# Kernel tuning notes

Hardware: AMD Instinct MI355X
Metric: run time of the kernel (lower is better)

The kernel has to match this reference:

```python
import jax, jax.numpy as jnp
import numpy as np
from jax import lax

DN = ('NHWC', 'HWIO', 'NHWC')

def conv2d_same(x, W, b):
    y = lax.conv_general_dilated(x, W, window_strides=(1, 1), padding='SAME', dimension_numbers=DN)
    return y + b

def maxpool2(x):
    # 2x2 max pool, stride 2, SAME padding (NHWC)
    return lax.reduce_window(x, -jnp.inf, lax.max, (1, 2, 2, 1), (1, 2, 2, 1), 'SAME')

def setup_inputs() -> dict:
    key = jax.random.key(0)
    ks = jax.random.split(key, 6)
    B, H, W, C = 8, 64, 64, 256
    s = 0.05
    return {
        'x': jax.random.normal(ks[0], (B, H, W, C), jnp.float32),
        'Wf': jax.random.normal(ks[1], (3, 3, C, C // 8), jnp.float32) * s,
        'bf': jnp.zeros((C // 8,), jnp.float32),
        'Wg': jax.random.normal(ks[2], (3, 3, C, C // 8), jnp.float32) * s,
        'bg': jnp.zeros((C // 8,), jnp.float32),
        'Wh': jax.random.normal(ks[3], (3, 3, C, C // 2), jnp.float32) * s,
        'bh': jnp.zeros((C // 2,), jnp.float32),
        'Wo': jax.random.normal(ks[4], (1, 1, C // 2, C), jnp.float32) * s,
        'bo': jnp.zeros((C,), jnp.float32),
        'gate': jnp.ones((1,), jnp.float32),
    }

def reference(x, Wf, bf, Wg, bg, Wh, bh, Wo, bo, gate):
    B, H, W, C = x.shape
    f = maxpool2(conv2d_same(x, Wf, bf))            # [B, H/2, W/2, C//8] keys
    g = conv2d_same(x, Wg, bg)                       # [B, H, W, C//8]     queries
    h = maxpool2(conv2d_same(x, Wh, bh))            # [B, H/2, W/2, C//2] values
    N, M = H * W, (H // 2) * (W // 2)
    gq = g.reshape(B, N, C // 8)
    fk = f.reshape(B, M, C // 8)
    hv = h.reshape(B, M, C // 2)
    attn = jax.nn.softmax(jnp.einsum('bnd,bmd->bnm', gq, fk), axis=-1)  # [B, N, M]
    wo = jnp.einsum('bnm,bmv->bnv', attn, hv).reshape(B, H, W, C // 2)
    out = conv2d_same(wo, Wo, bo)                    # [B, H, W, C]
    return x + gate[0] * out
```

## Files before the change

kernel.cpp:

```cpp
#include <hip/hip_runtime.h>
#include <hip/hip_fp16.h>

constexpr int B_  = 8;
constexpr int H_  = 64;
constexpr int W_  = 64;
constexpr int C_  = 256;
constexpr int CG_ = 32;
constexpr int CH_ = 128;
constexpr int NQ_ = 4096;
constexpr int NM_ = 1024;
constexpr int XP_ = 66;

constexpr int GP_ = 1048576;
constexpr int HP_ = 4194304;

typedef __attribute__((ext_vector_type(8))) _Float16 half8;
typedef __attribute__((ext_vector_type(4))) _Float16 half4;
typedef __attribute__((ext_vector_type(4))) float    f32x4;

__global__ void prep_w_k(const float* __restrict__ Wg, const float* __restrict__ Wf,
                         const float* __restrict__ Wh, const float* __restrict__ Wo,
                         const float* __restrict__ bg, const float* __restrict__ bf,
                         const float* __restrict__ bh,
                         _Float16* __restrict__ Wpk, _Float16* __restrict__ Wok,
                         float* __restrict__ bc) {
    int i = blockIdx.x * 256 + threadIdx.x;
    if (i < 12 * 9 * 8 * 64 * 8) {
        int j    = i & 7;
        int lane = (i >> 3) & 63;
        int ks   = (i >> 9) & 7;
        int tap  = (i >> 12) % 9;
        int co16 = i / 36864;
        int co = co16 * 16 + (lane & 15);
        int kk = tap * 256 + ks * 32 + (lane >> 4) * 8 + j;
        float v;
        if (co < 32)      v = Wg[(size_t)kk * 32  + co];
        else if (co < 64) v = Wf[(size_t)kk * 32  + (co - 32)];
        else              v = Wh[(size_t)kk * 128 + (co - 64)];
        Wpk[i] = (_Float16)v;
        return;
    }
    int i2 = i - 12 * 9 * 8 * 64 * 8;
    if (i2 < 16 * 4 * 64 * 8) {
        int j    = i2 & 7;
        int lane = (i2 >> 3) & 63;
        int ks   = (i2 >> 9) & 3;
        int co16 = i2 >> 11;
        int co = co16 * 16 + (lane & 15);
        int k  = ks * 32 + (lane >> 4) * 8 + j;
        Wok[i2] = (_Float16)Wo[(size_t)k * 256 + co];
        return;
    }
    int co = i2 - 16 * 4 * 64 * 8;
    if (co < 192)
        bc[co] = (co < 32) ? bg[co] : (co < 64) ? bf[co - 32] : bh[co - 64];
}

__global__ __launch_bounds__(256, 4) void conv_mfma_k(
        const float* __restrict__ X, const _Float16* __restrict__ Wpk,
        const float* __restrict__ bc,
        _Float16* __restrict__ gpart, _Float16* __restrict__ fpart,
        _Float16* __restrict__ hpart) {
    __shared__ char lds[XP_ * 256 * 2];
    int bid = blockIdx.x;
    int lg  = (bid & 7) * 192 + (bid >> 3);
    int ky  = lg % 3;
    int iy  = lg / 3;
    int b   = iy >> 6;
    int y   = iy & 63;
    int yy  = y + ky - 1;
    int tid = threadIdx.x;
    int wid = tid >> 6;
    int l   = tid & 63;
    int lr  = l & 15;
    int lk  = l >> 4;

    {
        bool rowok = (yy >= 0 && yy < 64);
        const float* xrow = X + ((size_t)(b * 64 + yy) * 64) * 256;
        half8 vst[9];
#pragma unroll
        for (int j = 0; j < 9; ++j) {
            int c = tid + j * 256;
            half8 v = (half8)(_Float16)0.f;
            if (j < 8 || tid < 64) {
                int px = c >> 5;
                int ch = (c & 31) * 8;
                if (rowok && px >= 1 && px <= 64) {
                    const float* s = xrow + (size_t)(px - 1) * 256 + ch;
                    float4 a  = *reinterpret_cast<const float4*>(s);
                    float4 b2 = *reinterpret_cast<const float4*>(s + 4);
                    v[0] = (_Float16)a.x;  v[1] = (_Float16)a.y;
                    v[2] = (_Float16)a.z;  v[3] = (_Float16)a.w;
                    v[4] = (_Float16)b2.x; v[5] = (_Float16)b2.y;
                    v[6] = (_Float16)b2.z; v[7] = (_Float16)b2.w;
                }
            }
            vst[j] = v;
        }
#pragma unroll
        for (int j = 0; j < 9; ++j) {
            int c = tid + j * 256;
            if (j < 8 || tid < 64) {
                int px = c >> 5;
                *reinterpret_cast<half8*>(lds + ((c * 16) ^ ((px & 7) << 4))) = vst[j];
            }
        }
    }
    __syncthreads();

    f32x4 acc[4][3];
#pragma unroll
    for (int mi = 0; mi < 4; ++mi)
#pragma unroll
        for (int nj = 0; nj < 3; ++nj) acc[mi][nj] = (f32x4)0.f;

    int tap0 = ky * 3;
    auto ldw = [&](int s, half8* d) {
        const _Float16* p = Wpk +
            ((((size_t)(wid * 3) * 9 + tap0 + (s >> 3)) * 8 + (s & 7)) * 64 + l) * 8;
        d[0] = *reinterpret_cast<const half8*>(p);
        d[1] = *reinterpret_cast<const half8*>(p + 36864);
        d[2] = *reinterpret_cast<const half8*>(p + 73728);
    };

    half8 wb[3][3];
    ldw(0, wb[0]);
    ldw(1, wb[1]);
#pragma unroll
    for (int st = 0; st < 24; ++st) {
        if (st < 22) ldw(st + 2, wb[(st + 2) % 3]);
        int kx = st >> 3, ks = st & 7;
        half8 af[4];
#pragma unroll
        for (int mi = 0; mi < 4; ++mi) {
            int px = mi * 16 + lr + kx;
            int ad = (px * 512 + ks * 64 + lk * 16) ^ ((px & 7) << 4);
            af[mi] = *reinterpret_cast<const half8*>(lds + ad);
        }
        const half8* w = wb[st % 3];
#pragma unroll
        for (int mi = 0; mi < 4; ++mi)
            acc[mi][0] = __builtin_amdgcn_mfma_f32_16x16x32_f16(af[mi], w[0], acc[mi][0], 0, 0, 0);
#pragma unroll
        for (int mi = 0; mi < 4; ++mi)
            acc[mi][1] = __builtin_amdgcn_mfma_f32_16x16x32_f16(af[mi], w[1], acc[mi][1], 0, 0, 0);
#pragma unroll
        for (int mi = 0; mi < 4; ++mi)
            acc[mi][2] = __builtin_amdgcn_mfma_f32_16x16x32_f16(af[mi], w[2], acc[mi][2], 0, 0, 0);
    }

    int pixbase = (b * 64 + y) * 64;
    bool addb = (ky == 1);
#pragma unroll
    for (int nj = 0; nj < 3; ++nj) {
        int co = wid * 48 + nj * 16 + lr;
        float bias = addb ? bc[co] : 0.f;
#pragma unroll
        for (int mi = 0; mi < 4; ++mi) {
#pragma unroll
            for (int r = 0; r < 4; ++r) {
                int x = mi * 16 + lk * 4 + r;
                float v = acc[mi][nj][r] + bias;
                size_t pix = pixbase + x;
                if (co < 32)
                    gpart[(size_t)ky * GP_ + pix * 32 + co] = (_Float16)(v * 1.44269504f);
                else if (co < 64)
                    fpart[(size_t)ky * GP_ + pix * 32 + (co - 32)] = (_Float16)v;
                else
                    hpart[(size_t)ky * HP_ + pix * 128 + (co - 64)] = (_Float16)v;
            }
        }
    }
}

__global__ void maxpool_f16_k(const _Float16* __restrict__ fp, _Float16* __restrict__ dst) {
    int i = blockIdx.x * 256 + threadIdx.x;
    if (i >= B_ * NM_ * CG_) return;
    int c = i & 31;
    int t = i >> 5;
    int px = t & 31;
    int py = (t >> 5) & 31;
    int b  = t >> 10;
    size_t base = (((size_t)(b * 64 + py * 2)) * 64 + px * 2) * 32 + c;
    const _Float16* p1 = fp + GP_;
    const _Float16* p2 = fp + 2 * GP_;
    auto val = [&](size_t o) { return (float)fp[o] + (float)p1[o] + (float)p2[o]; };
    float v = fmaxf(fmaxf(val(base), val(base + 32)),
                    fmaxf(val(base + 64 * 32), val(base + 64 * 32 + 32)));
    dst[i] = (_Float16)v;
}

__global__ __launch_bounds__(256) void vtpool_k(const _Float16* __restrict__ hp,
                                                _Float16* __restrict__ Vt) {
    __shared__ float t[32][33];
    int b  = blockIdx.x >> 7;
    int kt = (blockIdx.x >> 2) & 31;
    int ct = blockIdx.x & 3;
    int tid = threadIdx.x;
    const _Float16* p1 = hp + HP_;
    const _Float16* p2 = hp + 2 * (size_t)HP_;
#pragma unroll
    for (int i = 0; i < 4; ++i) {
        int e = tid + i * 256;
        int px = e >> 5, c = e & 31;
        size_t base = (((size_t)(b * 64 + kt * 2) * 64) + px * 2) * 128 + ct * 32 + c;
        auto val = [&](size_t o) { return (float)hp[o] + (float)p1[o] + (float)p2[o]; };
        float v = fmaxf(fmaxf(val(base), val(base + 128)),
                        fmaxf(val(base + 64 * 128), val(base + 64 * 128 + 128)));
        t[px][c] = v;
    }
    __syncthreads();
#pragma unroll
    for (int i = 0; i < 4; ++i) {
        int e = tid + i * 256;
        int c = e >> 5, px = e & 31;
        Vt[((size_t)b * 128 + ct * 32 + c) * 1024 + kt * 32 + px] = (_Float16)t[px][c];
    }
}

constexpr int PP_ = 72;

__global__ __launch_bounds__(256, 2) void attn_flash_k(
        const _Float16* __restrict__ Qp,
        const _Float16* __restrict__ Kf,
        const _Float16* __restrict__ Vt,
        _Float16* __restrict__ wo) {
    __shared__ _Float16 plds[4][16][PP_];
    __shared__ _Float16 vlds[2][8192];
    int bb  = blockIdx.x >> 6;
    int qt  = blockIdx.x & 63;
    int wid = threadIdx.x >> 6;
    int l   = threadIdx.x & 63;
    int lr  = l & 15;
    int lg  = l >> 4;
    int qbase = qt * 64 + wid * 16;

    const _Float16* gp = Qp + ((size_t)bb * NQ_ + qbase + lr) * 32 + lg * 8;
    half8 bq = *reinterpret_cast<const half8*>(gp);
    bq = bq + *reinterpret_cast<const half8*>(gp + GP_);
    bq = bq + *reinterpret_cast<const half8*>(gp + 2 * GP_);

    const _Float16* Kb = Kf + (size_t)bb * NM_ * 32;
    const _Float16* Vb = Vt + (size_t)bb * 128 * NM_;

    int o0  = wid * 4096 + l * 16;
    int vr0 = o0 >> 7;
    int vc  = (o0 >> 4) & 7;
    int vsw = (vr0 & 7) << 4;
    int lsw = (lr & 7) << 4;

    f32x4 acc[8];
#pragma unroll
    for (int vt = 0; vt < 8; ++vt) acc[vt] = (f32x4)0.f;
    float m_run = -1.0e30f;
    float l_lane = 0.f;

    half8 ak0, ak1, ak2, ak3;
    f32x4 s0, s1, s2, s3;
    half4 ph0, ph1, ph2, ph3;
    float4 vst[4];

#define STAGE_LOAD(T)                                                              \
    {   const _Float16* vp = Vb + (size_t)(T) * 64 + (size_t)vr0 * NM_ + vc * 8;   \
        vst[0] = *reinterpret_cast<const float4*>(vp);                             \
        vst[1] = *reinterpret_cast<const float4*>(vp + 8 * NM_);                   \
        vst[2] = *reinterpret_cast<const float4*>(vp + 16 * NM_);                  \
        vst[3] = *reinterpret_cast<const float4*>(vp + 24 * NM_);                  \
    }

#define STAGE_WRITE(BUF)                                                           \
    {   char* vbp = (char*)vlds[BUF] + (o0 ^ vsw);                                 \
        *reinterpret_cast<float4*>(vbp)        = vst[0];                           \
        *reinterpret_cast<float4*>(vbp + 1024) = vst[1];                           \
        *reinterpret_cast<float4*>(vbp + 2048) = vst[2];                           \
        *reinterpret_cast<float4*>(vbp + 3072) = vst[3];                           \
    }

#define LOADK(T)                                                                   \
    {   const _Float16* kp = Kb + (size_t)(T) * 64 * 32;                           \
        ak0 = *reinterpret_cast<const half8*>(kp + (size_t)(lr)      * 32 + lg*8); \
        ak1 = *reinterpret_cast<const half8*>(kp + (size_t)(16 + lr) * 32 + lg*8); \
        ak2 = *reinterpret_cast<const half8*>(kp + (size_t)(32 + lr) * 32 + lg*8); \
        ak3 = *reinterpret_cast<const half8*>(kp + (size_t)(48 + lr) * 32 + lg*8); \
    }

#define QK()                                                                \
    {   s0 = __builtin_amdgcn_mfma_f32_16x16x32_f16(ak0, bq, (f32x4)0.f, 0, 0, 0); \
        s1 = __builtin_amdgcn_mfma_f32_16x16x32_f16(ak1, bq, (f32x4)0.f, 0, 0, 0); \
        s2 = __builtin_amdgcn_mfma_f32_16x16x32_f16(ak2, bq, (f32x4)0.f, 0, 0, 0); \
        s3 = __builtin_amdgcn_mfma_f32_16x16x32_f16(ak3, bq, (f32x4)0.f, 0, 0, 0); \
    }

#define SOFTMAX()                                                           \
    {   float lm = fmaxf(fmaxf(fmaxf(s0[0], s0[1]), fmaxf(s0[2], s0[3])),   \
                         fmaxf(fmaxf(s1[0], s1[1]), fmaxf(s1[2], s1[3])));  \
        lm = fmaxf(lm, fmaxf(fmaxf(fmaxf(s2[0], s2[1]), fmaxf(s2[2], s2[3])), \
                             fmaxf(fmaxf(s3[0], s3[1]), fmaxf(s3[2], s3[3])))); \
        if (__any(lm > m_run + 11.0f)) {                                    \
            float mx = lm;                                                  \
            mx = fmaxf(mx, __shfl_xor(mx, 16, 64));                         \
            mx = fmaxf(mx, __shfl_xor(mx, 32, 64));                         \
            float mnew  = fmaxf(m_run, mx);                                 \
            float alpha = exp2f(m_run - mnew);                              \
            l_lane *= alpha;                                                \
            _Pragma("unroll")                                               \
            for (int r = 0; r < 4; ++r) {                                   \
                float ar = __shfl(alpha, 4 * lg + r, 64);                   \
                _Pragma("unroll")                                           \
                for (int vt = 0; vt < 8; ++vt) acc[vt][r] *= ar;            \
            }                                                               \
            m_run = mnew;                                                   \
        }                                                                   \
        float ps = 0.f;                                                     \
        {   float p0 = exp2f(s0[0]-m_run), p1 = exp2f(s0[1]-m_run);         \
            float p2 = exp2f(s0[2]-m_run), p3 = exp2f(s0[3]-m_run);         \
            ps += (p0+p1)+(p2+p3);                                          \
            ph0[0]=(_Float16)p0; ph0[1]=(_Float16)p1;                       \
            ph0[2]=(_Float16)p2; ph0[3]=(_Float16)p3; }                     \
        {   float p0 = exp2f(s1[0]-m_run), p1 = exp2f(s1[1]-m_run);         \
            float p2 = exp2f(s1[2]-m_run), p3 = exp2f(s1[3]-m_run);         \
            ps += (p0+p1)+(p2+p3);                                          \
            ph1[0]=(_Float16)p0; ph1[1]=(_Float16)p1;                       \
            ph1[2]=(_Float16)p2; ph1[3]=(_Float16)p3; }                     \
        {   float p0 = exp2f(s2[0]-m_run), p1 = exp2f(s2[1]-m_run);         \
            float p2 = exp2f(s2[2]-m_run), p3 = exp2f(s2[3]-m_run);         \
            ps += (p0+p1)+(p2+p3);                                          \
            ph2[0]=(_Float16)p0; ph2[1]=(_Float16)p1;                       \
            ph2[2]=(_Float16)p2; ph2[3]=(_Float16)p3; }                     \
        {   float p0 = exp2f(s3[0]-m_run), p1 = exp2f(s3[1]-m_run);         \
            float p2 = exp2f(s3[2]-m_run), p3 = exp2f(s3[3]-m_run);         \
            ps += (p0+p1)+(p2+p3);                                          \
            ph3[0]=(_Float16)p0; ph3[1]=(_Float16)p1;                       \
            ph3[2]=(_Float16)p2; ph3[3]=(_Float16)p3; }                     \
        l_lane += ps;                                                       \
    }

#define WRITEP()                                                            \
    {   *reinterpret_cast<half4*>(&plds[wid][lr][ 0 + 4*lg]) = ph0;         \
        *reinterpret_cast<half4*>(&plds[wid][lr][16 + 4*lg]) = ph1;         \
        *reinterpret_cast<half4*>(&plds[wid][lr][32 + 4*lg]) = ph2;         \
        *reinterpret_cast<half4*>(&plds[wid][lr][48 + 4*lg]) = ph3;         \
    }

#define PV(BUF)                                                             \
    {   half8 ap0 = *reinterpret_cast<const half8*>(&plds[wid][lr][8*lg]);  \
        half8 ap1 = *reinterpret_cast<const half8*>(&plds[wid][lr][32 + 8*lg]); \
        const char* vbp = (const char*)vlds[BUF];                           \
        _Pragma("unroll")                                                   \
        for (int vt = 0; vt < 8; ++vt) {                                    \
            int ra = (vt * 16 + lr) * 128;                                  \
            half8 bv = *reinterpret_cast<const half8*>(                     \
                vbp + ((ra + lg * 16) ^ lsw));                              \
            acc[vt] = __builtin_amdgcn_mfma_f32_16x16x32_f16(ap0, bv, acc[vt], 0, 0, 0); \
        }                                                                   \
        _Pragma("unroll")                                                   \
        for (int vt = 0; vt < 8; ++vt) {                                    \
            int ra = (vt * 16 + lr) * 128;                                  \
            half8 bv = *reinterpret_cast<const half8*>(                     \
                vbp + ((ra + (4 + lg) * 16) ^ lsw));                        \
            acc[vt] = __builtin_amdgcn_mfma_f32_16x16x32_f16(ap1, bv, acc[vt], 0, 0, 0); \
        }                                                                   \
    }

    STAGE_LOAD(0);
    STAGE_WRITE(0);
    LOADK(0);
    __syncthreads();
    QK(); SOFTMAX();

    for (int t = 0; t < 16; ++t) {
        if (t < 15) { STAGE_LOAD(t + 1); LOADK(t + 1); }
        WRITEP();
        PV(t & 1);
        if (t < 15) STAGE_WRITE((t + 1) & 1);
        __syncthreads();
        if (t < 15) { QK(); SOFTMAX(); }
    }

#undef STAGE_LOAD
#undef STAGE_WRITE
#undef LOADK
#undef QK
#undef SOFTMAX
#undef WRITEP
#undef PV

    float lsum = l_lane;
    lsum += __shfl_xor(lsum, 16, 64);
    lsum += __shfl_xor(lsum, 32, 64);
    float inv = 1.f / lsum;
#pragma unroll
    for (int r = 0; r < 4; ++r) {
        float ir = __shfl(inv, 4 * lg + r, 64);
        _Float16* orow = wo + ((size_t)bb * NQ_ + qbase + 4 * lg + r) * 128 + lr;
#pragma unroll
        for (int vt = 0; vt < 8; ++vt) orow[vt * 16] = (_Float16)(acc[vt][r] * ir);
    }
}

__global__ __launch_bounds__(256, 2) void conv1x1_mfma_k(
        const _Float16* __restrict__ wo, const _Float16* __restrict__ Wok,
        const float* __restrict__ bo, const float* __restrict__ X,
        const float* __restrict__ gate, float* __restrict__ out) {
    __shared__ char lds[64 * 256];
    int pix0 = blockIdx.x * 64;
    int tid = threadIdx.x;
    int wq = tid >> 6;
    int l  = tid & 63;
    int lr = l & 15;
    int lg = l >> 4;

    {
        const float4* sp = reinterpret_cast<const float4*>(wo + (size_t)pix0 * 128);
#pragma unroll
        for (int j = 0; j < 4; ++j) {
            int c = tid + j * 256;
            int px = c >> 4;
            *reinterpret_cast<float4*>(lds + ((c * 16) ^ ((px & 7) << 4))) = sp[c];
        }
    }
    __syncthreads();

    f32x4 acc[4][4];
#pragma unroll
    for (int mi = 0; mi < 4; ++mi)
#pragma unroll
        for (int nj = 0; nj < 4; ++nj) acc[mi][nj] = (f32x4)0.f;

#pragma unroll
    for (int ks = 0; ks < 4; ++ks) {
        half8 ap[4];
#pragma unroll
        for (int mi = 0; mi < 4; ++mi) {
            int px = mi * 16 + lr;
            int ad = (px * 256 + ks * 64 + lg * 16) ^ ((px & 7) << 4);
            ap[mi] = *reinterpret_cast<const half8*>(lds + ad);
        }
#pragma unroll
        for (int nj = 0; nj < 4; ++nj) {
            int co16 = wq * 4 + nj;
            half8 bv = *reinterpret_cast<const half8*>(
                Wok + (((size_t)co16 * 4 + ks) * 64 + l) * 8);
#pragma unroll
            for (int mi = 0; mi < 4; ++mi)
                acc[mi][nj] = __builtin_amdgcn_mfma_f32_16x16x32_f16(ap[mi], bv, acc[mi][nj], 0, 0, 0);
        }
    }

    float gt = gate[0];
#pragma unroll
    for (int nj = 0; nj < 4; ++nj) {
        int co = wq * 64 + nj * 16 + lr;
        float bias = bo[co];
#pragma unroll
        for (int mi = 0; mi < 4; ++mi) {
#pragma unroll
            for (int r = 0; r < 4; ++r) {
                size_t o = (size_t)(pix0 + mi * 16 + lg * 4 + r) * 256 + co;
                out[o] = X[o] + gt * (acc[mi][nj][r] + bias);
            }
        }
    }
}

extern "C" void kernel_launch(void* const* d_in, const int* in_sizes, int n_in,
                              void* d_out, int out_size, void* d_ws, size_t ws_size,
                              hipStream_t stream) {
    const float* X    = (const float*)d_in[0];
    const float* Wf   = (const float*)d_in[1];
    const float* bf   = (const float*)d_in[2];
    const float* Wg   = (const float*)d_in[3];
    const float* bg   = (const float*)d_in[4];
    const float* Wh   = (const float*)d_in[5];
    const float* bh   = (const float*)d_in[6];
    const float* Wo   = (const float*)d_in[7];
    const float* bo   = (const float*)d_in[8];
    const float* gate = (const float*)d_in[9];
    float* out = (float*)d_out;

    _Float16* gpart = (_Float16*)d_ws;
    _Float16* fpart = gpart + 3 * (size_t)GP_;
    _Float16* hpart = fpart + 3 * (size_t)GP_;
    _Float16* Kf    = hpart + 3 * (size_t)HP_;
    _Float16* Vt    = Kf + 262144;
    _Float16* Wpk   = Vt + 1048576;
    float*    bc    = (float*)(Wpk + 442368);
    _Float16* Wok   = (_Float16*)(bc + 192);
    _Float16* wobuf = hpart;

    prep_w_k<<<(12*9*8*64*8 + 16*4*64*8 + 192 + 255) / 256, 256, 0, stream>>>(
        Wg, Wf, Wh, Wo, bg, bf, bh, Wpk, Wok, bc);
    conv_mfma_k<<<3 * B_ * H_, 256, 0, stream>>>(X, Wpk, bc, gpart, fpart, hpart);
    maxpool_f16_k<<<(B_ * NM_ * CG_ + 255) / 256, 256, 0, stream>>>(fpart, Kf);
    vtpool_k<<<B_ * 32 * 4, 256, 0, stream>>>(hpart, Vt);
    attn_flash_k<<<B_ * 64, 256, 0, stream>>>(gpart, Kf, Vt, wobuf);
    conv1x1_mfma_k<<<(B_ * NQ_) / 64, 256, 0, stream>>>(wobuf, Wok, bo, X, gate, out);
}
```

Baseline: 107.9 us.

## Repartition conv MFMA warps by pixel strip instead of output-channel group

Each of the four waves now owns a 16-pixel strip and computes all 192 output channels (12 MFMA tiles), where before each wave owned 48 channels across all 64 pixels. This loads one A fragment per step from LDS instead of four, but every wave now loads all 12 weight fragments from global memory per step, without the previous software prefetch ring. The intent is to cut LDS traffic and balance register use. The risk is roughly four times more global/L2 weight traffic and exposed load latency.

New measurement: 201.1 us. 86.4% more time.

```diff
diff --git a/kernel.cpp b/kernel.cpp
--- a/kernel.cpp
+++ b/kernel.cpp
@@ -74,6 +74,7 @@
     int l   = tid & 63;
     int lr  = l & 15;
     int lk  = l >> 4;
+    int wbase = wid * 16;
 
     {
         bool rowok = (yy >= 0 && yy < 64);
@@ -109,67 +110,41 @@
     }
     __syncthreads();
 
-    f32x4 acc[4][3];
-#pragma unroll
-    for (int mi = 0; mi < 4; ++mi)
-#pragma unroll
-        for (int nj = 0; nj < 3; ++nj) acc[mi][nj] = (f32x4)0.f;
+    f32x4 acc[12];
+#pragma unroll
+    for (int c = 0; c < 12; ++c) acc[c] = (f32x4)0.f;
 
     int tap0 = ky * 3;
-    auto ldw = [&](int s, half8* d) {
-        const _Float16* p = Wpk +
-            ((((size_t)(wid * 3) * 9 + tap0 + (s >> 3)) * 8 + (s & 7)) * 64 + l) * 8;
-        d[0] = *reinterpret_cast<const half8*>(p);
-        d[1] = *reinterpret_cast<const half8*>(p + 36864);
-        d[2] = *reinterpret_cast<const half8*>(p + 73728);
-    };
-
-    half8 wb[3][3];
-    ldw(0, wb[0]);
-    ldw(1, wb[1]);
 #pragma unroll
     for (int st = 0; st < 24; ++st) {
-        if (st < 22) ldw(st + 2, wb[(st + 2) % 3]);
         int kx = st >> 3, ks = st & 7;
-        half8 af[4];
-#pragma unroll
-        for (int mi = 0; mi < 4; ++mi) {
-            int px = mi * 16 + lr + kx;
-            int ad = (px * 512 + ks * 64 + lk * 16) ^ ((px & 7) << 4);
-            af[mi] = *reinterpret_cast<const half8*>(lds + ad);
-        }
-        const half8* w = wb[st % 3];
-#pragma unroll
-        for (int mi = 0; mi < 4; ++mi)
-            acc[mi][0] = __builtin_amdgcn_mfma_f32_16x16x32_f16(af[mi], w[0], acc[mi][0], 0, 0, 0);
-#pragma unroll
-        for (int mi = 0; mi < 4; ++mi)
-            acc[mi][1] = __builtin_amdgcn_mfma_f32_16x16x32_f16(af[mi], w[1], acc[mi][1], 0, 0, 0);
-#pragma unroll
-        for (int mi = 0; mi < 4; ++mi)
-            acc[mi][2] = __builtin_amdgcn_mfma_f32_16x16x32_f16(af[mi], w[2], acc[mi][2], 0, 0, 0);
-    }
-
-    int pixbase = (b * 64 + y) * 64;
+        int px = wbase + lr + kx;
+        int ad = (px * 512 + ks * 64 + lk * 16) ^ ((px & 7) << 4);
+        half8 af = *reinterpret_cast<const half8*>(lds + ad);
+        const _Float16* wp = Wpk + ((size_t)(tap0 + kx) * 8 + ks) * 512 + l * 8;
+#pragma unroll
+        for (int c = 0; c < 12; ++c) {
+            half8 bf8 = *reinterpret_cast<const half8*>(wp + (size_t)c * 36864);
+            acc[c] = __builtin_amdgcn_mfma_f32_16x16x32_f16(af, bf8, acc[c], 0, 0, 0);
+        }
+    }
+
+    int pixbase = (b * 64 + y) * 64 + wbase;
     bool addb = (ky == 1);
 #pragma unroll
-    for (int nj = 0; nj < 3; ++nj) {
-        int co = wid * 48 + nj * 16 + lr;
+    for (int c = 0; c < 12; ++c) {
+        int co = c * 16 + lr;
         float bias = addb ? bc[co] : 0.f;
 #pragma unroll
-        for (int mi = 0; mi < 4; ++mi) {
-#pragma unroll
-            for (int r = 0; r < 4; ++r) {
-                int x = mi * 16 + lk * 4 + r;
-                float v = acc[mi][nj][r] + bias;
-                size_t pix = pixbase + x;
-                if (co < 32)
-                    gpart[(size_t)ky * GP_ + pix * 32 + co] = (_Float16)(v * 1.44269504f);
-                else if (co < 64)
-                    fpart[(size_t)ky * GP_ + pix * 32 + (co - 32)] = (_Float16)v;
-                else
-                    hpart[(size_t)ky * HP_ + pix * 128 + (co - 64)] = (_Float16)v;
-            }
+        for (int r = 0; r < 4; ++r) {
+            size_t pix = pixbase + lk * 4 + r;
+            float v = acc[c][r] + bias;
+            if (co < 32)
+                gpart[(size_t)ky * GP_ + pix * 32 + co] = (_Float16)(v * 1.44269504f);
+            else if (co < 64)
+                fpart[(size_t)ky * GP_ + pix * 32 + (co - 32)] = (_Float16)v;
+            else
+                hpart[(size_t)ky * HP_ + pix * 128 + (co - 64)] = (_Float16)v;
         }
     }
 }
```

## Process two output rows per conv block with 512 threads

Applied to the files above, without the earlier changes.

The 3x3 conv kernel now handles two adjacent output rows per block, using 8 waves where 4 split the output channels and 2 split the rows. Grid size halves while block size doubles, so weight fragments loaded from global memory are shared across both rows through cache. LDS padding columns are dropped in favour of clamped addresses plus zero masking at the image edges. The weight prefetch depth falls from two stages to one, which lowers register pressure but may expose more load latency. LDS use doubles to 64KB per block, which limits occupancy.

Result: faster. 105.1 us (-2.6%).

```diff
diff --git a/kernel.cpp b/kernel.cpp
--- a/kernel.cpp
+++ b/kernel.cpp
@@ -9,7 +9,6 @@
 constexpr int CH_ = 128;
 constexpr int NQ_ = 4096;
 constexpr int NM_ = 1024;
-constexpr int XP_ = 66;
 
 constexpr int GP_ = 1048576;
 constexpr int HP_ = 4194304;
@@ -56,55 +55,47 @@
         bc[co] = (co < 32) ? bg[co] : (co < 64) ? bf[co - 32] : bh[co - 64];
 }
 
-__global__ __launch_bounds__(256, 4) void conv_mfma_k(
+__global__ __launch_bounds__(512, 4) void conv_mfma_k(
         const float* __restrict__ X, const _Float16* __restrict__ Wpk,
         const float* __restrict__ bc,
         _Float16* __restrict__ gpart, _Float16* __restrict__ fpart,
         _Float16* __restrict__ hpart) {
-    __shared__ char lds[XP_ * 256 * 2];
+    __shared__ char lds[2 * 32768];
     int bid = blockIdx.x;
-    int lg  = (bid & 7) * 192 + (bid >> 3);
+    int lg  = (bid & 7) * 96 + (bid >> 3);
     int ky  = lg % 3;
-    int iy  = lg / 3;
-    int b   = iy >> 6;
-    int y   = iy & 63;
-    int yy  = y + ky - 1;
+    int ip  = lg / 3;
+    int b   = ip >> 5;
+    int y0  = (ip & 31) * 2;
     int tid = threadIdx.x;
     int wid = tid >> 6;
+    int rid = wid >> 2;
+    int nw  = wid & 3;
     int l   = tid & 63;
     int lr  = l & 15;
     int lk  = l >> 4;
 
     {
-        bool rowok = (yy >= 0 && yy < 64);
-        const float* xrow = X + ((size_t)(b * 64 + yy) * 64) * 256;
-        half8 vst[9];
-#pragma unroll
-        for (int j = 0; j < 9; ++j) {
-            int c = tid + j * 256;
+#pragma unroll
+        for (int j = 0; j < 8; ++j) {
+            int cc  = tid + j * 512;
+            int row = cc >> 11;
+            int c   = cc & 2047;
+            int px  = c >> 5;
+            int c8  = (c & 31) * 8;
+            int yin = y0 + ky - 1 + row;
             half8 v = (half8)(_Float16)0.f;
-            if (j < 8 || tid < 64) {
-                int px = c >> 5;
-                int ch = (c & 31) * 8;
-                if (rowok && px >= 1 && px <= 64) {
-                    const float* s = xrow + (size_t)(px - 1) * 256 + ch;
-                    float4 a  = *reinterpret_cast<const float4*>(s);
-                    float4 b2 = *reinterpret_cast<const float4*>(s + 4);
-                    v[0] = (_Float16)a.x;  v[1] = (_Float16)a.y;
-                    v[2] = (_Float16)a.z;  v[3] = (_Float16)a.w;
-                    v[4] = (_Float16)b2.x; v[5] = (_Float16)b2.y;
-                    v[6] = (_Float16)b2.z; v[7] = (_Float16)b2.w;
-                }
+            if (yin >= 0 && yin < 64) {
+                const float* s = X + (((size_t)(b * 64 + yin) * 64) + px) * 256 + c8;
+                float4 a  = *reinterpret_cast<const float4*>(s);
+                float4 b2 = *reinterpret_cast<const float4*>(s + 4);
+                v[0] = (_Float16)a.x;  v[1] = (_Float16)a.y;
+                v[2] = (_Float16)a.z;  v[3] = (_Float16)a.w;
+                v[4] = (_Float16)b2.x; v[5] = (_Float16)b2.y;
+                v[6] = (_Float16)b2.z; v[7] = (_Float16)b2.w;
             }
-            vst[j] = v;
-        }
-#pragma unroll
-        for (int j = 0; j < 9; ++j) {
-            int c = tid + j * 256;
-            if (j < 8 || tid < 64) {
-                int px = c >> 5;
-                *reinterpret_cast<half8*>(lds + ((c * 16) ^ ((px & 7) << 4))) = vst[j];
-            }
+            *reinterpret_cast<half8*>(lds + row * 32768 +
+                ((c * 16) ^ ((px & 7) << 4))) = v;
         }
     }
     __syncthreads();
@@ -116,29 +107,33 @@
         for (int nj = 0; nj < 3; ++nj) acc[mi][nj] = (f32x4)0.f;
 
     int tap0 = ky * 3;
+    const char* ldsr = lds + rid * 32768;
+
     auto ldw = [&](int s, half8* d) {
         const _Float16* p = Wpk +
-            ((((size_t)(wid * 3) * 9 + tap0 + (s >> 3)) * 8 + (s & 7)) * 64 + l) * 8;
+            ((((size_t)(nw * 3) * 9 + tap0 + (s >> 3)) * 8 + (s & 7)) * 64 + l) * 8;
         d[0] = *reinterpret_cast<const half8*>(p);
         d[1] = *reinterpret_cast<const half8*>(p + 36864);
         d[2] = *reinterpret_cast<const half8*>(p + 73728);
     };
 
-    half8 wb[3][3];
+    half8 wb[2][3];
     ldw(0, wb[0]);
-    ldw(1, wb[1]);
 #pragma unroll
     for (int st = 0; st < 24; ++st) {
-        if (st < 22) ldw(st + 2, wb[(st + 2) % 3]);
+        if (st < 23) ldw(st + 1, wb[(st + 1) & 1]);
         int kx = st >> 3, ks = st & 7;
         half8 af[4];
 #pragma unroll
         for (int mi = 0; mi < 4; ++mi) {
-            int px = mi * 16 + lr + kx;
-            int ad = (px * 512 + ks * 64 + lk * 16) ^ ((px & 7) << 4);
-            af[mi] = *reinterpret_cast<const half8*>(lds + ad);
-        }
-        const half8* w = wb[st % 3];
+            int px  = mi * 16 + lr + kx - 1;
+            int pxc = px < 0 ? 0 : (px > 63 ? 63 : px);
+            int ad  = (pxc * 512 + ks * 64 + lk * 16) ^ ((pxc & 7) << 4);
+            half8 a = *reinterpret_cast<const half8*>(ldsr + ad);
+            if (px < 0 || px > 63) a = (half8)(_Float16)0.f;
+            af[mi] = a;
+        }
+        const half8* w = wb[st & 1];
 #pragma unroll
         for (int mi = 0; mi < 4; ++mi)
             acc[mi][0] = __builtin_amdgcn_mfma_f32_16x16x32_f16(af[mi], w[0], acc[mi][0], 0, 0, 0);
@@ -150,11 +145,11 @@
             acc[mi][2] = __builtin_amdgcn_mfma_f32_16x16x32_f16(af[mi], w[2], acc[mi][2], 0, 0, 0);
     }
 
-    int pixbase = (b * 64 + y) * 64;
+    int pixbase = (b * 64 + y0 + rid) * 64;
     bool addb = (ky == 1);
 #pragma unroll
     for (int nj = 0; nj < 3; ++nj) {
-        int co = wid * 48 + nj * 16 + lr;
+        int co = nw * 48 + nj * 16 + lr;
         float bias = addb ? bc[co] : 0.f;
 #pragma unroll
         for (int mi = 0; mi < 4; ++mi) {
@@ -491,7 +486,7 @@
 
     prep_w_k<<<(12*9*8*64*8 + 16*4*64*8 + 192 + 255) / 256, 256, 0, stream>>>(
         Wg, Wf, Wh, Wo, bg, bf, bh, Wpk, Wok, bc);
-    conv_mfma_k<<<3 * B_ * H_, 256, 0, stream>>>(X, Wpk, bc, gpart, fpart, hpart);
+    conv_mfma_k<<<3 * B_ * 32, 512, 0, stream>>>(X, Wpk, bc, gpart, fpart, hpart);
     maxpool_f16_k<<<(B_ * NM_ * CG_ + 255) / 256, 256, 0, stream>>>(fpart, Kf);
     vtpool_k<<<B_ * 32 * 4, 256, 0, stream>>>(hpart, Vt);
     attn_flash_k<<<B_ * 64, 256, 0, stream>>>(gpart, Kf, Vt, wobuf);
```
